# Kernel optimization log

Hardware: AMD Instinct MI355X
Metric: run time of the kernel (lower is better)

## Reference

```python
import jax, jax.numpy as jnp
import numpy as np

N = 10000   # nodes (cells)
E = 100000  # edges
G = 2000    # num_genes
H = 20      # heads
C1 = 128    # layer-1 out channels per head
C2 = 128    # latent_dim
NEG_SLOPE = 0.2


def setup_inputs():
    key = jax.random.key(0)
    ks = jax.random.split(key, 9)
    s = 0.05
    return {
        "x": jax.random.normal(ks[0], (N, G), jnp.float32),
        "edge_index": jax.random.randint(ks[1], (2, E), 0, N, dtype=jnp.int64),
        "W1": jax.random.normal(ks[2], (G, H * C1), jnp.float32) * s,
        "att_src1": jax.random.normal(ks[3], (H, C1), jnp.float32) * s,
        "att_dst1": jax.random.normal(ks[4], (H, C1), jnp.float32) * s,
        "b1": jnp.zeros((H * C1,), jnp.float32),
        "W2": jax.random.normal(ks[5], (H * C1, H * C2), jnp.float32) * s,
        "att_src2": jax.random.normal(ks[6], (H, C2), jnp.float32) * s,
        "att_dst2": jax.random.normal(ks[7], (H, C2), jnp.float32) * s,
        "b2": jnp.zeros((C2,), jnp.float32),
    }


def _gat_conv(x, W, att_src, att_dst, bias, src, dst, concat):
    """PyG GATConv (eval mode, self-loops already in src/dst)."""
    n = x.shape[0]
    h_, c_ = att_src.shape
    h = (x @ W).reshape(n, h_, c_)                      # [N, H, C]
    a_src = jnp.einsum("nhc,hc->nh", h, att_src)        # [N, H]
    a_dst = jnp.einsum("nhc,hc->nh", h, att_dst)        # [N, H]
    e = a_src[src] + a_dst[dst]                          # [E, H]
    e = jnp.where(e > 0, e, NEG_SLOPE * e)               # leaky_relu
    # segment softmax over incoming edges of each destination node
    e_max = jax.ops.segment_max(e, dst, num_segments=n)  # [N, H]
    ex = jnp.exp(e - e_max[dst])                         # [E, H]
    denom = jax.ops.segment_sum(ex, dst, num_segments=n)
    alpha = ex / denom[dst]                              # [E, H]
    msg = alpha[:, :, None] * h[src]                     # [E, H, C]
    out = jax.ops.segment_sum(msg, dst, num_segments=n)  # [N, H, C]
    if concat:
        out = out.reshape(n, h_ * c_)
    else:
        out = out.mean(axis=1)                           # [N, C]
    return out + bias


def reference(x, edge_index, W1, att_src1, att_dst1, b1, W2, att_src2, att_dst2, b2):
    n = x.shape[0]
    loop = jnp.arange(n, dtype=edge_index.dtype)
    src = jnp.concatenate([edge_index[0], loop])  # PyG add_self_loops=True
    dst = jnp.concatenate([edge_index[1], loop])
    h1 = _gat_conv(x, W1, att_src1, att_dst1, b1, src, dst, concat=True)
    h1 = jax.nn.relu(h1)  # dropout is identity in eval mode
    h2 = _gat_conv(h1, W2, att_src2, att_dst2, b2, src, dst, concat=False)
    return jax.nn.relu(h2)
```

## Files before the change

### kernel.cpp

```cpp
#include <hip/hip_runtime.h>

#define NEG_SLOPE 0.2f

typedef __attribute__((ext_vector_type(4))) float floatx4;
typedef __attribute__((ext_vector_type(8))) short shortx8;

__device__ __forceinline__ unsigned short f2bf(float f) {
  union { float f; unsigned int u; } v;
  v.f = f;
  unsigned int r = (v.u + 0x7FFFu + ((v.u >> 16) & 1u)) >> 16;
  return (unsigned short)r;
}
__device__ __forceinline__ float bf2f(unsigned short u) {
  union { unsigned int u; float f; } v;
  v.u = (unsigned int)u << 16;
  return v.f;
}
__device__ __forceinline__ void store_out(float* p, float v) { *p = v; }
__device__ __forceinline__ void store_out(unsigned short* p, float v) { *p = f2bf(v); }

__device__ __forceinline__ void gload_lds16(const unsigned short* g, unsigned short* l) {
  __builtin_amdgcn_global_load_lds(
      (const __attribute__((address_space(1))) void*)(g),
      (__attribute__((address_space(3))) void*)(l), 16, 0, 0);
}

__device__ __forceinline__ int load_edge(const void* ei, long idx, int is64) {
  if (is64) return (int)((const long long*)ei)[idx];
  return ((const int*)ei)[idx];
}

__global__ void detect64_kernel(const unsigned int* __restrict__ p, int* __restrict__ flag) {
  int is64 = 1;
  for (int i = 0; i < 32; ++i)
    if (p[2 * i + 1] != 0u) is64 = 0;
  *flag = is64;
}

__global__ void init_cnt_kernel(int* __restrict__ cnt, int n) {
  int i = blockIdx.x * blockDim.x + threadIdx.x;
  if (i < n) cnt[i] = 1;
}

__global__ void count_kernel(const void* __restrict__ ei, const int* __restrict__ flag, int E,
                             int* __restrict__ cnt) {
  int e = blockIdx.x * blockDim.x + threadIdx.x;
  if (e >= E) return;
  int is64 = *flag;
  int d = load_edge(ei, (long)E + e, is64);
  atomicAdd(&cnt[d], 1);
}

__global__ __launch_bounds__(1024) void scan_kernel(const int* __restrict__ cnt,
                                                    int* __restrict__ offs, int n) {
  __shared__ int partial[1024];
  int t = threadIdx.x;
  int per = (n + 1023) / 1024;
  int beg = t * per;
  int end = min(beg + per, n);
  int sum = 0;
  for (int i = beg; i < end; ++i) sum += cnt[i];
  partial[t] = sum;
  __syncthreads();
  for (int d = 1; d < 1024; d <<= 1) {
    int v = (t >= d) ? partial[t - d] : 0;
    __syncthreads();
    partial[t] += v;
    __syncthreads();
  }
  int excl = (t == 0) ? 0 : partial[t - 1];
  for (int i = beg; i < end; ++i) { offs[i] = excl; excl += cnt[i]; }
  if (t == 1023) offs[n] = partial[1023];
}

__global__ void init_self_kernel(const int* __restrict__ offs, int* __restrict__ srcs,
                                 int* __restrict__ fill, int n) {
  int i = blockIdx.x * blockDim.x + threadIdx.x;
  if (i < n) { srcs[offs[i]] = i; fill[i] = 1; }
}

__global__ void scatter_kernel(const void* __restrict__ ei, const int* __restrict__ flag, int E,
                               const int* __restrict__ offs, int* __restrict__ fill,
                               int* __restrict__ srcs) {
  int e = blockIdx.x * blockDim.x + threadIdx.x;
  if (e >= E) return;
  int is64 = *flag;
  int s = load_edge(ei, e, is64);
  int d = load_edge(ei, (long)E + e, is64);
  int pos = offs[d] + atomicAdd(&fill[d], 1);
  srcs[pos] = s;
}


__global__ __launch_bounds__(256) void pack_a_kernel(const float* __restrict__ in,
                                                     unsigned short* __restrict__ out, int M,
                                                     int K, int Kpad) {
  int rt = blockIdx.x;
  int r = threadIdx.x & 127;
  int kq = threadIdx.x >> 7;
  int row = rt * 128 + r;
  int nkc = Kpad >> 3;
  unsigned short* obase = out + (long)rt * Kpad * 128 + r * 8;
  const float* irow = in + (long)row * K;
  for (int kc = kq + (int)blockIdx.y * 2; kc < nkc; kc += (int)gridDim.y * 2) {
    int k = kc << 3;
    shortx8 o;
    if (row < M && k + 8 <= K && (K & 3) == 0) {
      float4 v0 = *(const float4*)(irow + k);
      float4 v1 = *(const float4*)(irow + k + 4);
      o[0] = (short)f2bf(v0.x); o[1] = (short)f2bf(v0.y);
      o[2] = (short)f2bf(v0.z); o[3] = (short)f2bf(v0.w);
      o[4] = (short)f2bf(v1.x); o[5] = (short)f2bf(v1.y);
      o[6] = (short)f2bf(v1.z); o[7] = (short)f2bf(v1.w);
    } else {
#pragma unroll
      for (int i = 0; i < 8; ++i) {
        int kk = k + i;
        float v = (row < M && kk < K) ? irow[kk] : 0.f;
        o[i] = (short)f2bf(v);
      }
    }
    *(shortx8*)(obase + (long)kc * 1024) = o;
  }
}

__global__ __launch_bounds__(256) void transpose_pack_kernel(const float* __restrict__ in,
                                                             unsigned short* __restrict__ out,
                                                             int K, int N, int Kpad) {
  __shared__ float tile[32][33];
  int kb = blockIdx.x * 32;
  int nb = blockIdx.y * 32;
  int tx = threadIdx.x & 31;
  int ty = threadIdx.x >> 5;
#pragma unroll
  for (int i = 0; i < 32; i += 8) {
    int k = kb + ty + i;
    tile[ty + i][tx] = (k < K) ? in[(long)k * N + nb + tx] : 0.f;
  }
  __syncthreads();
  if (threadIdx.x < 128) {
    int nl = threadIdx.x & 31;
    int nn = nb + nl;
    int kc4 = threadIdx.x >> 5;
    int k0 = kc4 * 8;
    shortx8 o;
#pragma unroll
    for (int j = 0; j < 8; ++j) o[j] = (short)f2bf(tile[k0 + j][nl]);
    int kc = (kb >> 3) + kc4;
    *(shortx8*)(out + (long)(nn >> 7) * Kpad * 128 + (long)kc * 1024 + (nn & 127) * 8) = o;
  }
}

template <typename OT>
__global__ __launch_bounds__(256) void mfma_gemm_kernel(const unsigned short* __restrict__ A,
                                                        const unsigned short* __restrict__ Bt,
                                                        OT* __restrict__ C, int M, int N, int K) {
  __shared__ unsigned short As[3][4096];
  __shared__ unsigned short Bs[3][4096];

  int tid = threadIdx.x;
  int lane = tid & 63;
  int w = tid >> 6;
  int wm = w & 1, wn = w >> 1;
  int bn = blockIdx.x * 128;
  int bm = blockIdx.y * 128;
  int quad = lane >> 4, l16 = lane & 15;

  const unsigned short* pA = A + (long)(bm >> 7) * K * 128 + tid * 8;
  const unsigned short* pB = Bt + (long)(bn >> 7) * K * 128 + tid * 8;
  unsigned short* la = &As[0][0] + w * 512;
  unsigned short* lb = &Bs[0][0] + w * 512;

  floatx4 acc[4][4];
#pragma unroll
  for (int i = 0; i < 4; ++i)
#pragma unroll
    for (int j = 0; j < 4; ++j) acc[i][j] = (floatx4){0.f, 0.f, 0.f, 0.f};

  int nk = K >> 5;
  gload_lds16(pA, la);
  gload_lds16(pA + 2048, la + 2048);
  gload_lds16(pB, lb);
  gload_lds16(pB + 2048, lb + 2048);
  if (nk > 1) {
    gload_lds16(pA + 4096, la + 4096);
    gload_lds16(pA + 4096 + 2048, la + 4096 + 2048);
    gload_lds16(pB + 4096, lb + 4096);
    gload_lds16(pB + 4096 + 2048, lb + 4096 + 2048);
  }

  int cur = 0, st = 2;
  for (int k = 0; k < nk; ++k) {
    if (k + 2 < nk) {
      const unsigned short* qA = pA + (long)(k + 2) * 4096;
      const unsigned short* qB = pB + (long)(k + 2) * 4096;
      unsigned short* da = la + st * 4096;
      unsigned short* db = lb + st * 4096;
      gload_lds16(qA, da);
      gload_lds16(qA + 2048, da + 2048);
      gload_lds16(qB, db);
      gload_lds16(qB + 2048, db + 2048);
      __builtin_amdgcn_s_waitcnt(0x0F78);
    } else if (k + 1 < nk) {
      __builtin_amdgcn_s_waitcnt(0x0F74);
    } else {
      __builtin_amdgcn_s_waitcnt(0x0F70);
    }
    __builtin_amdgcn_s_barrier();

    shortx8 a[4], b[4];
#pragma unroll
    for (int i = 0; i < 4; ++i) {
      a[i] = *(const shortx8*)(&As[cur][(quad * 128 + wm * 64 + i * 16 + l16) * 8]);
      b[i] = *(const shortx8*)(&Bs[cur][(quad * 128 + wn * 64 + i * 16 + l16) * 8]);
    }
#pragma unroll
    for (int i = 0; i < 4; ++i)
#pragma unroll
      for (int j = 0; j < 4; ++j)
        acc[i][j] = __builtin_amdgcn_mfma_f32_16x16x32_bf16(a[i], b[j], acc[i][j], 0, 0, 0);

    __builtin_amdgcn_s_barrier();
    cur = (cur == 2) ? 0 : cur + 1;
    st = (st == 2) ? 0 : st + 1;
  }

  int orow0 = bm + wm * 64 + quad * 4;
  int ocol0 = bn + wn * 64 + l16;
#pragma unroll
  for (int i = 0; i < 4; ++i)
#pragma unroll
    for (int j = 0; j < 4; ++j)
#pragma unroll
      for (int r2 = 0; r2 < 4; ++r2) {
        int rr = orow0 + i * 16 + r2;
        if (rr < M) store_out(&C[(long)rr * N + ocol0 + j * 16], acc[i][j][r2]);
      }
}

__global__ __launch_bounds__(256) void att_coef_kernel(const unsigned short* __restrict__ h,
                                                       const float* __restrict__ att_s,
                                                       const float* __restrict__ att_d,
                                                       float* __restrict__ a_s,
                                                       float* __restrict__ a_d, int n, int H,
                                                       int C) {
  int wave = (int)((blockIdx.x * blockDim.x + threadIdx.x) >> 6);
  int lane = threadIdx.x & 63;
  if (wave >= n) return;
  const unsigned short* row = h + (long)wave * H * C;
  for (int hh = 0; hh < H; ++hh) {
    float s = 0.f, d = 0.f;
    for (int c = lane; c < C; c += 64) {
      float v = bf2f(row[hh * C + c]);
      s += v * att_s[hh * C + c];
      d += v * att_d[hh * C + c];
    }
#pragma unroll
    for (int o = 32; o > 0; o >>= 1) {
      s += __shfl_down(s, o, 64);
      d += __shfl_down(d, o, 64);
    }
    if (lane == 0) {
      a_s[(long)wave * H + hh] = s;
      a_d[(long)wave * H + hh] = d;
    }
  }
}

__global__ void edge_softmax_kernel(const float* __restrict__ a_src,
                                    const float* __restrict__ a_dst,
                                    const int* __restrict__ offs, const int* __restrict__ srcs,
                                    float* __restrict__ alpha, int n, int H) {
  int idx = blockIdx.x * blockDim.x + threadIdx.x;
  if (idx >= n * H) return;
  int dstn = idx / H;
  int hh = idx - dstn * H;
  int beg = offs[dstn], end = offs[dstn + 1];
  float ad = a_dst[idx];
  float m = -1e30f;
  for (int j = beg; j < end; ++j) {
    float e = a_src[srcs[j] * H + hh] + ad;
    e = e > 0.f ? e : NEG_SLOPE * e;
    m = fmaxf(m, e);
  }
  float ssum = 0.f;
  for (int j = beg; j < end; ++j) {
    float e = a_src[srcs[j] * H + hh] + ad;
    e = e > 0.f ? e : NEG_SLOPE * e;
    float ex = __expf(e - m);
    alpha[(long)j * H + hh] = ex;
    ssum += ex;
  }
  float inv = 1.f / ssum;
  for (int j = beg; j < end; ++j) alpha[(long)j * H + hh] *= inv;
}

__global__ __launch_bounds__(320) void aggregate1_kernel(const unsigned short* __restrict__ h,
                                                         const float* __restrict__ alpha,
                                                         const int* __restrict__ offs,
                                                         const int* __restrict__ srcs,
                                                         const float* __restrict__ bias,
                                                         unsigned short* __restrict__ out, int H,
                                                         int C, int HC) {
  int dstn = blockIdx.x;
  int t = threadIdx.x;
  int beg = offs[dstn], end = offs[dstn + 1];
  int nf8 = HC >> 3;
  for (int fid = t; fid < nf8; fid += blockDim.x) {
    int hh = (fid << 3) / C;
    float acc[8];
#pragma unroll
    for (int i = 0; i < 8; ++i) acc[i] = 0.f;
    for (int j = beg; j < end; ++j) {
      int s = srcs[j];
      float al = alpha[(long)j * H + hh];
      shortx8 r = ((const shortx8*)(h + (long)s * HC))[fid];
#pragma unroll
      for (int i = 0; i < 8; ++i) acc[i] = fmaf(al, bf2f((unsigned short)r[i]), acc[i]);
    }
    shortx8 o;
#pragma unroll
    for (int i = 0; i < 8; ++i) {
      float bb = bias[(fid << 3) + i];
      o[i] = (short)f2bf(fmaxf(acc[i] + bb, 0.f));
    }
    *(shortx8*)(out + (long)(dstn >> 7) * HC * 128 + (long)fid * 1024 + (dstn & 127) * 8) = o;
  }
}

__global__ __launch_bounds__(128) void aggregate2_kernel(const unsigned short* __restrict__ h,
                                                         const float* __restrict__ alpha,
                                                         const int* __restrict__ offs,
                                                         const int* __restrict__ srcs,
                                                         const float* __restrict__ bias,
                                                         float* __restrict__ out, int H, int C) {
  int dstn = blockIdx.x;
  int c = threadIdx.x;
  if (c >= C) return;
  int beg = offs[dstn], end = offs[dstn + 1];
  int HC = H * C;
  float acc = 0.f;
  for (int j = beg; j < end; ++j) {
    int s = srcs[j];
    const unsigned short* row = h + (long)s * HC;
    const float* al = alpha + (long)j * H;
#pragma unroll 5
    for (int hh = 0; hh < H; ++hh) acc = fmaf(al[hh], bf2f(row[hh * C + c]), acc);
  }
  float v = acc * (1.f / (float)H) + bias[c];
  out[(long)dstn * C + c] = v > 0.f ? v : 0.f;
}

static inline size_t align256(size_t x) { return (x + 255) & ~(size_t)255; }

extern "C" void kernel_launch(void* const* d_in, const int* in_sizes, int n_in, void* d_out,
                              int out_size, void* d_ws, size_t ws_size, hipStream_t stream) {
  const float* x        = (const float*)d_in[0];
  const void*  ei       = d_in[1];
  const float* W1       = (const float*)d_in[2];
  const float* att_src1 = (const float*)d_in[3];
  const float* att_dst1 = (const float*)d_in[4];
  const float* b1       = (const float*)d_in[5];
  const float* W2       = (const float*)d_in[6];
  const float* att_src2 = (const float*)d_in[7];
  const float* att_dst2 = (const float*)d_in[8];
  const float* b2       = (const float*)d_in[9];
  float* out = (float*)d_out;

  const int C2  = in_sizes[9];
  const int H   = in_sizes[7] / C2;
  const int HC1 = in_sizes[5];
  const int C1  = HC1 / H;
  const int G   = in_sizes[2] / HC1;
  const int Nn  = in_sizes[0] / G;
  const int E   = in_sizes[1] / 2;
  const int HC2 = H * C2;
  const int Et  = E + Nn;
  const int Mpad = ((Nn + 127) / 128) * 128;
  const int K1pad = ((G + 31) / 32) * 32;

  char* p = (char*)d_ws;
  size_t off = 0;
  unsigned short* hb  = (unsigned short*)(p + off); off = align256(off + (size_t)Mpad * (HC1 > HC2 ? HC1 : HC2) * 2);
  unsigned short* xb  = (unsigned short*)(p + off); off = align256(off + (size_t)Mpad * K1pad * 2);
  unsigned short* xb2 = (unsigned short*)(p + off); off = align256(off + (size_t)Mpad * HC1 * 2);
  unsigned short* W1t = (unsigned short*)(p + off); off = align256(off + (size_t)HC1 * K1pad * 2);
  unsigned short* W2t = (unsigned short*)(p + off); off = align256(off + (size_t)HC2 * HC1 * 2);
  float* a_s   = (float*)(p + off); off = align256(off + (size_t)Nn * H * 4);
  float* a_d   = (float*)(p + off); off = align256(off + (size_t)Nn * H * 4);
  float* alpha = (float*)(p + off); off = align256(off + (size_t)Et * H * 4);
  int* cnt     = (int*)(p + off); off = align256(off + (size_t)Nn * 4);
  int* offs    = (int*)(p + off); off = align256(off + (size_t)(Nn + 1) * 4);
  int* fill    = (int*)(p + off); off = align256(off + (size_t)Nn * 4);
  int* srcs    = (int*)(p + off); off = align256(off + (size_t)Et * 4);
  int* flag64  = (int*)(p + off); off = align256(off + 16);
  (void)ws_size; (void)n_in; (void)out_size;

  const int TB = 256;
  detect64_kernel<<<1, 1, 0, stream>>>((const unsigned int*)ei, flag64);
  init_cnt_kernel<<<(Nn + TB - 1) / TB, TB, 0, stream>>>(cnt, Nn);
  count_kernel<<<(E + TB - 1) / TB, TB, 0, stream>>>(ei, flag64, E, cnt);
  scan_kernel<<<1, 1024, 0, stream>>>(cnt, offs, Nn);
  init_self_kernel<<<(Nn + TB - 1) / TB, TB, 0, stream>>>(offs, srcs, fill, Nn);
  scatter_kernel<<<(E + TB - 1) / TB, TB, 0, stream>>>(ei, flag64, E, offs, fill, srcs);

  {
    dim3 ga(Mpad / 128, 8);
    pack_a_kernel<<<ga, 256, 0, stream>>>(x, xb, Nn, G, K1pad);
    dim3 g1(K1pad / 32, HC1 / 32);
    transpose_pack_kernel<<<g1, 256, 0, stream>>>(W1, W1t, G, HC1, K1pad);
    dim3 g2(HC1 / 32, HC2 / 32);
    transpose_pack_kernel<<<g2, 256, 0, stream>>>(W2, W2t, HC1, HC2, HC1);
  }

  {
    dim3 grid(HC1 / 128, Mpad / 128);
    mfma_gemm_kernel<unsigned short><<<grid, 256, 0, stream>>>(xb, W1t, hb, Nn, HC1, K1pad);
  }
  att_coef_kernel<<<(Nn + 3) / 4, 256, 0, stream>>>(hb, att_src1, att_dst1, a_s, a_d, Nn, H, C1);
  edge_softmax_kernel<<<(Nn * H + TB - 1) / TB, TB, 0, stream>>>(a_s, a_d, offs, srcs, alpha, Nn, H);
  aggregate1_kernel<<<Nn, 320, 0, stream>>>(hb, alpha, offs, srcs, b1, xb2, H, C1, HC1);

  {
    dim3 grid(HC2 / 128, Mpad / 128);
    mfma_gemm_kernel<unsigned short><<<grid, 256, 0, stream>>>(xb2, W2t, hb, Nn, HC2, HC1);
  }
  att_coef_kernel<<<(Nn + 3) / 4, 256, 0, stream>>>(hb, att_src2, att_dst2, a_s, a_d, Nn, H, C2);
  edge_softmax_kernel<<<(Nn * H + TB - 1) / TB, TB, 0, stream>>>(a_s, a_d, offs, srcs, alpha, Nn, H);
  aggregate2_kernel<<<Nn, 128, 0, stream>>>(hb, alpha, offs, srcs, b2, out, H, C2);
}
```

Measured before the change: 876.1 us.

## Parallelize layer-2 aggregation across heads with vectorized loads and LDS reduction

The layer-2 aggregation kernel now uses 256 threads per destination node. Each thread loads 8 bf16 channels with a single vector load and covers up to two heads, so heads are split across thread groups instead of looped serially by each thread. Per-group partial sums go through shared memory and are reduced before the mean, bias and ReLU. This targets the serial head loop and the scalar 2-byte loads, at the cost of a shared-memory reduction and a block barrier, and it assumes C is a power of two with H no larger than twice the number of head groups.

```diff
diff --git a/kernel.cpp b/kernel.cpp
--- a/kernel.cpp
+++ b/kernel.cpp
@@ -328,27 +328,53 @@
   }
 }
 
-__global__ __launch_bounds__(128) void aggregate2_kernel(const unsigned short* __restrict__ h,
+__global__ __launch_bounds__(256) void aggregate2_kernel(const unsigned short* __restrict__ h,
                                                          const float* __restrict__ alpha,
                                                          const int* __restrict__ offs,
                                                          const int* __restrict__ srcs,
                                                          const float* __restrict__ bias,
                                                          float* __restrict__ out, int H, int C) {
+  __shared__ float smem[16 * 256];
   int dstn = blockIdx.x;
-  int c = threadIdx.x;
-  if (c >= C) return;
+  int t = threadIdx.x;
+  int HC = H * C;
+  int nc8 = C >> 3;
+  int c8 = t & (nc8 - 1);
+  int hgrp = t >> __builtin_ctz(nc8);
+  int nHgrp = 256 >> __builtin_ctz(nc8);
   int beg = offs[dstn], end = offs[dstn + 1];
-  int HC = H * C;
-  float acc = 0.f;
+
+  float acc[2][8];
+#pragma unroll
+  for (int hi = 0; hi < 2; ++hi)
+#pragma unroll
+    for (int i = 0; i < 8; ++i) acc[hi][i] = 0.f;
+
   for (int j = beg; j < end; ++j) {
     int s = srcs[j];
     const unsigned short* row = h + (long)s * HC;
     const float* al = alpha + (long)j * H;
-#pragma unroll 5
-    for (int hh = 0; hh < H; ++hh) acc = fmaf(al[hh], bf2f(row[hh * C + c]), acc);
-  }
-  float v = acc * (1.f / (float)H) + bias[c];
-  out[(long)dstn * C + c] = v > 0.f ? v : 0.f;
+#pragma unroll
+    for (int hi = 0; hi < 2; ++hi) {
+      int hh = hgrp + hi * nHgrp;
+      if (hh < H) {
+        float a = al[hh];
+        shortx8 r = *(const shortx8*)(row + hh * C + c8 * 8);
+#pragma unroll
+        for (int i = 0; i < 8; ++i) acc[hi][i] = fmaf(a, bf2f((unsigned short)r[i]), acc[hi][i]);
+      }
+    }
+  }
+#pragma unroll
+  for (int i = 0; i < 8; ++i) smem[hgrp * C + c8 * 8 + i] = acc[0][i] + acc[1][i];
+  __syncthreads();
+  float invH = 1.f / (float)H;
+  for (int c = t; c < C; c += 256) {
+    float s = 0.f;
+    for (int g = 0; g < nHgrp; ++g) s += smem[g * C + c];
+    float v = s * invH + bias[c];
+    out[(long)dstn * C + c] = v > 0.f ? v : 0.f;
+  }
 }
 
 static inline size_t align256(size_t x) { return (x + 255) & ~(size_t)255; }
@@ -427,5 +453,5 @@
   }
   att_coef_kernel<<<(Nn + 3) / 4, 256, 0, stream>>>(hb, att_src2, att_dst2, a_s, a_d, Nn, H, C2);
   edge_softmax_kernel<<<(Nn * H + TB - 1) / TB, TB, 0, stream>>>(a_s, a_d, offs, srcs, alpha, Nn, H);
-  aggregate2_kernel<<<Nn, 128, 0, stream>>>(hb, alpha, offs, srcs, b2, out, H, C2);
-}
+  aggregate2_kernel<<<Nn, 256, 0, stream>>>(hb, alpha, offs, srcs, b2, out, H, C2);
+}
```

After: 869.5 us. About the same (-0.8%).
